# Kernel optimization log

Hardware: AMD Instinct MI355X
Metric: run time of the kernel (lower is better)

Reference implementation:

```python
import jax, jax.numpy as jnp
import numpy as np

DIM = 384
HEADS = 12
K = 3          # kernel_size
PAD = 1
STRIDE = 1
B, H, W = 8, 56, 56


def conv1x1(x, w, b=None):
    # x: [B,C,H,W], w: [O,C]
    y = jnp.einsum('bchw,oc->bohw', x, w)
    if b is not None:
        y = y + b[None, :, None, None]
    return y


def unfold(x, k, p, s):
    # torch nn.Unfold: returns patches [B, C, k*k, nH, nW], kernel row-major, channel-major overall
    Bx, C, Hx, Wx = x.shape
    nH = (Hx + 2 * p - k) // s + 1
    nW = (Wx + 2 * p - k) // s + 1
    xp = jnp.pad(x, ((0, 0), (0, 0), (p, p), (p, p)))
    cols = [xp[:, :, i:i + s * nH:s, j:j + s * nW:s] for i in range(k) for j in range(k)]
    return jnp.stack(cols, axis=2), nH, nW


def fold(col, Hx, Wx, k, p, s):
    # torch F.fold (col2im): scatter-add overlapping windows. col: [B, C, k*k, nH, nW]
    Bx, C, _, nH, nW = col.shape
    canvas = jnp.zeros((Bx, C, Hx + 2 * p, Wx + 2 * p), col.dtype)
    idx = 0
    for i in range(k):
        for j in range(k):
            canvas = canvas.at[:, :, i:i + s * nH:s, j:j + s * nW:s].add(col[:, :, idx])
            idx += 1
    return canvas[:, :, p:p + Hx, p:p + Wx]


def setup_inputs() -> dict:
    key = jax.random.key(0)
    ks = jax.random.split(key, 5)
    k2 = K * K
    x = jax.random.normal(ks[0], (B, DIM, H, W), dtype=jnp.float32)
    v_w = jax.random.normal(ks[1], (DIM, DIM), dtype=jnp.float32) * 0.02
    v_b = jnp.zeros((DIM,), dtype=jnp.float32)
    attn_w = jax.random.normal(ks[2], (k2 * k2 * HEADS, DIM), dtype=jnp.float32) * 0.02
    proj_w = jax.random.normal(ks[3], (DIM, DIM), dtype=jnp.float32) * 0.02
    return {'x': x, 'v_w': v_w, 'v_b': v_b, 'attn_w': attn_w, 'proj_w': proj_w}


def reference(x, v_w, v_b, attn_w, proj_w):
    Bx, C, Hx, Wx = x.shape
    k2 = K * K
    hd = C // HEADS  # head dim
    # value projection + unfold into overlapping k x k windows
    v = conv1x1(x, v_w, v_b)
    vcol, nH, nW = unfold(v, K, PAD, STRIDE)        # [B, C, k2, nH, nW]
    L = nH * nW
    v = vcol.reshape(Bx, HEADS, hd, k2, L)          # split C = (heads, hd), heads slow
    v = v.transpose(0, 1, 4, 3, 2)                  # [B, n, L, k2(d), hd]
    # adaptive avg pool to (nH, nW); with stride=1 this is identity (pool window 1)
    ph, pw = Hx // nH, Wx // nW
    xp = x.reshape(Bx, C, nH, ph, nW, pw).mean(axis=(3, 5))
    # per-pixel attention logits, channel layout = ((i*k2 + d)*HEADS + head)
    a = jnp.einsum('bchw,oc->bohw', xp, attn_w)     # [B, k2*k2*n, nH, nW]
    a = a.reshape(Bx, k2, k2, HEADS, L)             # [B, i, d, n, L]
    a = a.transpose(0, 3, 4, 1, 2)                  # [B, n, L, i, d]
    a = jax.nn.softmax(a, axis=-1)
    out = jnp.einsum('bnlid,bnldh->bnlih', a, v)    # [B, n, L, i, hd]
    out = out.transpose(0, 1, 4, 3, 2)              # [B, n, hd, i, L] -> channel (n*hd+h)
    out = out.reshape(Bx, C, k2, nH, nW)
    out = fold(out, Hx, Wx, K, PAD, STRIDE)         # scatter-add windows back
    return conv1x1(out, proj_w)
```

## Files before the change

### kernel.cpp

```cpp
#include <hip/hip_runtime.h>
#include <hip/hip_bf16.h>

#define DIM   384
#define HEADS 12
#define K2    9
#define HH    56
#define WW    56
#define HWP   3136
#define BB    8
#define AO    972
#define AOP   1024
#define MCAT  1408
#define PP    3200

typedef __hip_bfloat16 bf16;
typedef short bf16x8 __attribute__((ext_vector_type(8)));
typedef short bf16x4v __attribute__((ext_vector_type(4)));
typedef float f32x4 __attribute__((ext_vector_type(4)));

static __device__ __forceinline__ float b2f(bf16 v) { return __bfloat162float(v); }
static __device__ __forceinline__ float bs2f(short s) {
    return __uint_as_float(((unsigned int)(unsigned short)s) << 16);
}
static __device__ __forceinline__ short f2bs(float f) {
    __hip_bfloat16 h = __float2bfloat16(f);
    return *(short*)&h;
}

static __device__ __forceinline__ void gl_lds16(const bf16* g, bf16* l) {
    __builtin_amdgcn_global_load_lds(
        (const __attribute__((address_space(1))) unsigned int*)g,
        (__attribute__((address_space(3))) unsigned int*)l, 16, 0, 0);
}

__global__ __launch_bounds__(256) void prep_kernel(
        const float* __restrict__ x, const float* __restrict__ v_w,
        const float* __restrict__ attn_w, const float* __restrict__ proj_w,
        bf16* __restrict__ xT, bf16* __restrict__ wcat, bf16* __restrict__ wp) {
    const int bid = blockIdx.x;
    if (bid < 400) {
        const int lane = threadIdx.x & 63, w = threadIdx.x >> 6;
        const int p = (bid % 50) * 64 + lane;
        const int b = bid / 50;
        bf16* dst = xT + ((size_t)b * PP + p) * DIM;
        if (p >= HWP) {
            bf16x8 z = {};
            for (int cg = w; cg < 48; cg += 4) *(bf16x8*)(dst + cg * 8) = z;
            return;
        }
        const float* src = x + (size_t)b * DIM * HWP + p;
        for (int cg = w; cg < 48; cg += 4) {
            bf16x8 v;
#pragma unroll
            for (int j = 0; j < 8; j++) v[j] = f2bs(src[(size_t)(cg * 8 + j) * HWP]);
            *(bf16x8*)(dst + cg * 8) = v;
        }
    } else {
        const int idx = (bid - 400) * 256 + threadIdx.x;
        const int NCAT = MCAT * DIM;
        if (idx < NCAT) {
            const int row = idx / DIM, col = idx % DIM;
            float v;
            if (row < 384) v = v_w[row * DIM + col];
            else { const int r2 = row - 384; v = (r2 < AO) ? attn_w[r2 * DIM + col] : 0.f; }
            *(short*)&wcat[idx] = f2bs(v);
        } else {
            const int j = idx - NCAT;
            if (j < 384 * DIM) *(short*)&wp[j] = f2bs(proj_w[j]);
        }
    }
}

#define GEMM_MAIN_LOOP_V4(Ab, Bb, lA, lB, acc)                                 \
    for (int k0 = 0; k0 < DIM; k0 += 64) {                                     \
        _Pragma("unroll")                                                      \
        for (int r = 0; r < 4; r++) {                                          \
            int idx = r * 256 + t;                                             \
            int row = idx >> 3;                                                \
            int kq = ((idx & 7) - (row >> 1)) & 7;                             \
            gl_lds16(Ab + (size_t)row * DIM + k0 + kq * 8, lA + idx * 8);      \
        }                                                                      \
        _Pragma("unroll")                                                      \
        for (int r = 0; r < 4; r++) {                                          \
            int idx = r * 256 + t;                                             \
            int row = idx >> 3;                                                \
            int kq = ((idx & 7) - (row >> 1)) & 7;                             \
            gl_lds16(Bb + (size_t)row * DIM + k0 + kq * 8, lB + idx * 8);      \
        }                                                                      \
        __syncthreads();                                                       \
        _Pragma("unroll")                                                      \
        for (int h = 0; h < 2; h++) {                                          \
            const int swzh = (((h << 2) + quad + (l16 >> 1)) & 7) * 8;         \
            bf16x8 af[4], bfr[4];                                              \
            _Pragma("unroll")                                                  \
            for (int mt = 0; mt < 4; mt++)                                     \
                af[mt] = *(const bf16x8*)(lA + (wm * 64 + mt * 16 + l16) * 64 + swzh); \
            _Pragma("unroll")                                                  \
            for (int nt = 0; nt < 4; nt++)                                     \
                bfr[nt] = *(const bf16x8*)(lB + (wn * 64 + nt * 16 + l16) * 64 + swzh); \
            _Pragma("unroll")                                                  \
            for (int mt = 0; mt < 4; mt++)                                     \
                _Pragma("unroll")                                              \
                for (int nt = 0; nt < 4; nt++)                                 \
                    acc[mt][nt] = __builtin_amdgcn_mfma_f32_16x16x32_bf16(     \
                        af[mt], bfr[nt], acc[mt][nt], 0, 0, 0);                \
        }                                                                      \
        __syncthreads();                                                       \
    }

__global__ __launch_bounds__(256) void gemm12_kernel(
        const bf16* __restrict__ A, const bf16* __restrict__ Bt,
        const float* __restrict__ bias, bf16* __restrict__ vT,
        bf16* __restrict__ lT) {
    __shared__ bf16 lds[16384];
    bf16* lA = lds;
    bf16* lB = lds + 8192;
    const int t = threadIdx.x;
    const int lane = t & 63, w = t >> 6;
    const int wm = w & 1, wn = w >> 1;
    const int quad = lane >> 4, l16 = lane & 15;
    const int n0 = blockIdx.x * 128;
    const int m0 = blockIdx.y * 128;
    const int b = blockIdx.z;

    const bf16* Ab = A + (size_t)m0 * DIM;
    const bf16* Bb = Bt + ((size_t)b * PP + n0) * DIM;

    f32x4 acc[4][4] = {};
    GEMM_MAIN_LOOP_V4(Ab, Bb, lA, lB, acc)

    const bool isv = (m0 < 384);
    bf16* outp = isv ? vT : lT;
    const int ostr = isv ? DIM : AOP;
    const int ch0 = isv ? m0 : m0 - 384;

    bf16* wbuf = lds + w * 1152;
    const int nr = lane >> 2;
    const int mc = (lane & 3) * 16;
#pragma unroll
    for (int nt = 0; nt < 4; nt++) {
#pragma unroll
        for (int mt = 0; mt < 4; mt++) {
            float4 bi = make_float4(0.f, 0.f, 0.f, 0.f);
            if (isv) bi = *(const float4*)(bias + ch0 + wm * 64 + mt * 16 + quad * 4);
            bf16x4v pk;
            pk[0] = f2bs(acc[mt][nt][0] + bi.x);
            pk[1] = f2bs(acc[mt][nt][1] + bi.y);
            pk[2] = f2bs(acc[mt][nt][2] + bi.z);
            pk[3] = f2bs(acc[mt][nt][3] + bi.w);
            *(bf16x4v*)(wbuf + l16 * 72 + mt * 16 + quad * 4) = pk;
        }
        bf16x8 v0 = *(const bf16x8*)(wbuf + nr * 72 + mc);
        bf16x8 v1 = *(const bf16x8*)(wbuf + nr * 72 + mc + 8);
        const int p = n0 + wn * 64 + nt * 16 + nr;
        if (p < HWP) {
            bf16* dp = outp + ((size_t)b * PP + p) * ostr + ch0 + wm * 64 + mc;
            *(bf16x8*)dp = v0;
            *(bf16x8*)(dp + 8) = v1;
        }
    }
}

__global__ __launch_bounds__(256) void gemm_planar_kernel(
        const bf16* __restrict__ A, const bf16* __restrict__ Bt,
        float* __restrict__ out) {
    __shared__ bf16 lds[16384];
    bf16* lA = lds;
    bf16* lB = lds + 8192;
    const int t = threadIdx.x;
    const int lane = t & 63, w = t >> 6;
    const int wm = w & 1, wn = w >> 1;
    const int quad = lane >> 4, l16 = lane & 15;
    const int n0 = blockIdx.x * 128;
    const int m0 = blockIdx.y * 128;
    const int b = blockIdx.z;

    const bf16* Ab = A + (size_t)m0 * DIM;
    const bf16* Bb = Bt + ((size_t)b * PP + n0) * DIM;

    f32x4 acc[4][4] = {};
    GEMM_MAIN_LOOP_V4(Ab, Bb, lA, lB, acc)

#pragma unroll
    for (int mt = 0; mt < 4; mt++) {
#pragma unroll
        for (int nt = 0; nt < 4; nt++) {
            int p = n0 + wn * 64 + nt * 16 + l16;
            if (p >= HWP) continue;
#pragma unroll
            for (int reg = 0; reg < 4; reg++) {
                int o = m0 + wm * 64 + mt * 16 + quad * 4 + reg;
                out[((size_t)b * DIM + o) * HWP + p] = acc[mt][nt][reg];
            }
        }
    }
}

__global__ __launch_bounds__(384) void attn_fold_kernel(
        const bf16* __restrict__ lT, const bf16* __restrict__ vT,
        bf16* __restrict__ cT) {
    __shared__ bf16 P[8 * 9 * 12 * 9];
    __shared__ float Wf[8 * 25 * 12];
    const int t = threadIdx.x;
    const int b = blockIdx.y;
    const int pix0 = blockIdx.x * 8;
    const int Y = pix0 / WW, X0 = pix0 % WW;

    for (int r = t; r < 864; r += 384) {
        const int px = r / 108, rem = r % 108;
        const int i = rem / 12, n = rem % 12;
        const int ir = i / 3, ic = i % 3;
        const int yi = Y + 1 - ir, xi = X0 + px + 1 - ic;
        bf16* Pd = &P[r * 9];
        if (yi < 0 || yi >= HH || xi < 0 || xi >= WW) {
#pragma unroll
            for (int d = 0; d < K2; d++) *(short*)&Pd[d] = 0;
        } else {
            const bf16* base = lT + ((size_t)b * PP + yi * WW + xi) * AOP + i * 108 + n;
            float lv[K2];
            float m = -1e30f;
#pragma unroll
            for (int d = 0; d < K2; d++) {
                lv[d] = b2f(base[d * 12]);
                m = fmaxf(m, lv[d]);
            }
            float s = 0.f;
#pragma unroll
            for (int d = 0; d < K2; d++) { lv[d] = __expf(lv[d] - m); s += lv[d]; }
            const float inv = 1.f / s;
#pragma unroll
            for (int d = 0; d < K2; d++) *(short*)&Pd[d] = f2bs(lv[d] * inv);
        }
    }
    __syncthreads();

    for (int e = t; e < 2400; e += 384) {
        const int px = e / 300, rem = e % 300;
        const int off = rem / 12, n = rem % 12;
        const int dy = off / 5 - 2, dx = off % 5 - 2;
        const int ir_lo = max(0, -dy), ir_hi = min(2, 2 - dy);
        const int ic_lo = max(0, -dx), ic_hi = min(2, 2 - dx);
        float wsum = 0.f;
        for (int ir = ir_lo; ir <= ir_hi; ir++)
            for (int ic = ic_lo; ic <= ic_hi; ic++) {
                const int i = ir * 3 + ic;
                const int d = (dy + ir) * 3 + (dx + ic);
                wsum += b2f(P[((px * 9 + i) * 12 + n) * 9 + d]);
            }
        Wf[e] = wsum;
    }
    __syncthreads();

    const int px = t / 48, cg = t % 48;
    const int X = X0 + px;
    const int n = cg >> 2;
    const float* Wp = &Wf[px * 300];
    const bf16* vb = vT + (size_t)b * PP * DIM;
    float acc[8] = {};
#pragma unroll
    for (int dy = -2; dy <= 2; dy++) {
        const int ny = Y + dy;
        if (ny < 0 || ny >= HH) continue;
#pragma unroll
        for (int dx = -2; dx <= 2; dx++) {
            const int nx = X + dx;
            const bool ok = (nx >= 0 && nx < WW);
            const int nxc = min(max(nx, 0), WW - 1);
            const float w = ok ? Wp[((dy + 2) * 5 + dx + 2) * 12 + n] : 0.f;
            bf16x8 vv = *(const bf16x8*)(vb + (size_t)(ny * WW + nxc) * DIM + cg * 8);
#pragma unroll
            for (int j = 0; j < 8; j++) acc[j] += w * bs2f(vv[j]);
        }
    }
    bf16x8 po;
#pragma unroll
    for (int j = 0; j < 8; j++) po[j] = f2bs(acc[j]);
    *(bf16x8*)(cT + ((size_t)b * PP + pix0 + px) * DIM + cg * 8) = po;
}

extern "C" void kernel_launch(void* const* d_in, const int* in_sizes, int n_in,
                              void* d_out, int out_size, void* d_ws, size_t ws_size,
                              hipStream_t stream) {
    const float* x      = (const float*)d_in[0];
    const float* v_w    = (const float*)d_in[1];
    const float* v_b    = (const float*)d_in[2];
    const float* attn_w = (const float*)d_in[3];
    const float* proj_w = (const float*)d_in[4];
    float* out = (float*)d_out;

    bf16* xT    = (bf16*)d_ws;
    bf16* vT    = xT + (size_t)BB * PP * DIM;
    bf16* lT    = vT + (size_t)BB * PP * DIM;
    bf16* wcat  = lT + (size_t)BB * PP * AOP;
    bf16* wp    = wcat + (size_t)MCAT * DIM;
    bf16* cT    = xT;

    const int NW = MCAT * DIM + 384 * DIM;
    const int nprep = 400 + (NW + 255) / 256;
    prep_kernel<<<nprep, 256, 0, stream>>>(x, v_w, attn_w, proj_w, xT, wcat, wp);

    gemm12_kernel<<<dim3(PP / 128, MCAT / 128, BB), 256, 0, stream>>>(wcat, xT, v_b, vT, lT);
    attn_fold_kernel<<<dim3(HWP / 8, BB), 384, 0, stream>>>(lT, vT, cT);
    gemm_planar_kernel<<<dim3(PP / 128, 3, BB), 256, 0, stream>>>(wp, cT, out);
}
```

Measured before the change: 217.8 us.

## Store value tensor in zero-padded 60x60 layout to remove fold boundary checks

```diff
diff --git a/kernel.cpp b/kernel.cpp
--- a/kernel.cpp
+++ b/kernel.cpp
@@ -12,11 +12,17 @@
 #define AOP   1024
 #define MCAT  1408
 #define PP    3200
+#define PPAD  3600
+#define W60   60
+
+#define WBLK     2688
+#define HALOBLK  696
 
 typedef __hip_bfloat16 bf16;
 typedef short bf16x8 __attribute__((ext_vector_type(8)));
 typedef short bf16x4v __attribute__((ext_vector_type(4)));
 typedef float f32x4 __attribute__((ext_vector_type(4)));
+typedef float f32x2 __attribute__((ext_vector_type(2)));
 
 static __device__ __forceinline__ float b2f(bf16 v) { return __bfloat162float(v); }
 static __device__ __forceinline__ float bs2f(short s) {
@@ -25,6 +31,12 @@
 static __device__ __forceinline__ short f2bs(float f) {
     __hip_bfloat16 h = __float2bfloat16(f);
     return *(short*)&h;
+}
+static __device__ __forceinline__ f32x2 unpk(unsigned int u) {
+    f32x2 r;
+    r[0] = __uint_as_float(u << 16);
+    r[1] = __uint_as_float(u & 0xffff0000u);
+    return r;
 }
 
 static __device__ __forceinline__ void gl_lds16(const bf16* g, bf16* l) {
@@ -36,7 +48,8 @@
 __global__ __launch_bounds__(256) void prep_kernel(
         const float* __restrict__ x, const float* __restrict__ v_w,
         const float* __restrict__ attn_w, const float* __restrict__ proj_w,
-        bf16* __restrict__ xT, bf16* __restrict__ wcat, bf16* __restrict__ wp) {
+        bf16* __restrict__ xT, bf16* __restrict__ wcat, bf16* __restrict__ wp,
+        bf16* __restrict__ vP) {
     const int bid = blockIdx.x;
     if (bid < 400) {
         const int lane = threadIdx.x & 63, w = threadIdx.x >> 6;
@@ -55,7 +68,7 @@
             for (int j = 0; j < 8; j++) v[j] = f2bs(src[(size_t)(cg * 8 + j) * HWP]);
             *(bf16x8*)(dst + cg * 8) = v;
         }
-    } else {
+    } else if (bid < 400 + WBLK) {
         const int idx = (bid - 400) * 256 + threadIdx.x;
         const int NCAT = MCAT * DIM;
         if (idx < NCAT) {
@@ -68,6 +81,24 @@
             const int j = idx - NCAT;
             if (j < 384 * DIM) *(short*)&wp[j] = f2bs(proj_w[j]);
         }
+    } else {
+        const int hidx = (bid - 400 - WBLK) * 256 + threadIdx.x;
+        const int b = hidx / 22272;
+        const int r = hidx % 22272;
+        const int hp = r / 48, cgi = r % 48;
+        int row, col;
+        if (hp < 240) {
+            const int rr = hp / 60;
+            row = (rr < 2) ? rr : rr + 56;
+            col = hp % 60;
+        } else {
+            const int h2 = hp - 240;
+            row = 2 + (h2 >> 2);
+            const int c4 = h2 & 3;
+            col = (c4 < 2) ? c4 : c4 + 56;
+        }
+        bf16x8 z = {};
+        *(bf16x8*)(vP + ((size_t)b * PPAD + row * W60 + col) * DIM + cgi * 8) = z;
     }
 }
 
@@ -110,7 +141,7 @@
 
 __global__ __launch_bounds__(256) void gemm12_kernel(
         const bf16* __restrict__ A, const bf16* __restrict__ Bt,
-        const float* __restrict__ bias, bf16* __restrict__ vT,
+        const float* __restrict__ bias, bf16* __restrict__ vP,
         bf16* __restrict__ lT) {
     __shared__ bf16 lds[16384];
     bf16* lA = lds;
@@ -130,8 +161,6 @@
     GEMM_MAIN_LOOP_V4(Ab, Bb, lA, lB, acc)
 
     const bool isv = (m0 < 384);
-    bf16* outp = isv ? vT : lT;
-    const int ostr = isv ? DIM : AOP;
     const int ch0 = isv ? m0 : m0 - 384;
 
     bf16* wbuf = lds + w * 1152;
@@ -154,7 +183,13 @@
         bf16x8 v1 = *(const bf16x8*)(wbuf + nr * 72 + mc + 8);
         const int p = n0 + wn * 64 + nt * 16 + nr;
         if (p < HWP) {
-            bf16* dp = outp + ((size_t)b * PP + p) * ostr + ch0 + wm * 64 + mc;
+            bf16* dp;
+            if (isv) {
+                const int y = p / WW;
+                dp = vP + ((size_t)b * PPAD + p + y * 4 + 122) * DIM + ch0 + wm * 64 + mc;
+            } else {
+                dp = lT + ((size_t)b * PP + p) * AOP + ch0 + wm * 64 + mc;
+            }
             *(bf16x8*)dp = v0;
             *(bf16x8*)(dp + 8) = v1;
         }
@@ -197,7 +232,7 @@
 }
 
 __global__ __launch_bounds__(384) void attn_fold_kernel(
-        const bf16* __restrict__ lT, const bf16* __restrict__ vT,
+        const bf16* __restrict__ lT, const bf16* __restrict__ vP,
         bf16* __restrict__ cT) {
     __shared__ bf16 P[8 * 9 * 12 * 9];
     __shared__ float Wf[8 * 25 * 12];
@@ -234,47 +269,52 @@
     }
     __syncthreads();
 
-    for (int e = t; e < 2400; e += 384) {
-        const int px = e / 300, rem = e % 300;
-        const int off = rem / 12, n = rem % 12;
+    if (t < 300) {
+        const int off = t / 12, n = t % 12;
         const int dy = off / 5 - 2, dx = off % 5 - 2;
         const int ir_lo = max(0, -dy), ir_hi = min(2, 2 - dy);
         const int ic_lo = max(0, -dx), ic_hi = min(2, 2 - dx);
-        float wsum = 0.f;
-        for (int ir = ir_lo; ir <= ir_hi; ir++)
-            for (int ic = ic_lo; ic <= ic_hi; ic++) {
-                const int i = ir * 3 + ic;
-                const int d = (dy + ir) * 3 + (dx + ic);
-                wsum += b2f(P[((px * 9 + i) * 12 + n) * 9 + d]);
-            }
-        Wf[e] = wsum;
+#pragma unroll
+        for (int px = 0; px < 8; px++) {
+            float wsum = 0.f;
+            for (int ir = ir_lo; ir <= ir_hi; ir++)
+                for (int ic = ic_lo; ic <= ic_hi; ic++) {
+                    const int i = ir * 3 + ic;
+                    const int d = (dy + ir) * 3 + (dx + ic);
+                    wsum += b2f(P[((px * 9 + i) * 12 + n) * 9 + d]);
+                }
+            Wf[(px * 25 + off) * 12 + n] = wsum;
+        }
     }
     __syncthreads();
 
     const int px = t / 48, cg = t % 48;
     const int X = X0 + px;
     const int n = cg >> 2;
-    const float* Wp = &Wf[px * 300];
-    const bf16* vb = vT + (size_t)b * PP * DIM;
-    float acc[8] = {};
+    const float* Wp = &Wf[px * 300 + n];
+    const bf16* vbp = vP + ((size_t)b * PPAD + (size_t)(Y + 2) * W60 + (X + 2)) * DIM + cg * 8;
+    f32x2 a2[4] = {};
 #pragma unroll
     for (int dy = -2; dy <= 2; dy++) {
-        const int ny = Y + dy;
-        if (ny < 0 || ny >= HH) continue;
+        const bf16* rowb = vbp + dy * (W60 * DIM);
+        const float* wrow = Wp + (dy + 2) * 60;
 #pragma unroll
         for (int dx = -2; dx <= 2; dx++) {
-            const int nx = X + dx;
-            const bool ok = (nx >= 0 && nx < WW);
-            const int nxc = min(max(nx, 0), WW - 1);
-            const float w = ok ? Wp[((dy + 2) * 5 + dx + 2) * 12 + n] : 0.f;
-            bf16x8 vv = *(const bf16x8*)(vb + (size_t)(ny * WW + nxc) * DIM + cg * 8);
-#pragma unroll
-            for (int j = 0; j < 8; j++) acc[j] += w * bs2f(vv[j]);
+            const float w = wrow[(dx + 2) * 12];
+            const uint4 d = *(const uint4*)(rowb + dx * DIM);
+            f32x2 w2; w2[0] = w; w2[1] = w;
+            a2[0] = __builtin_elementwise_fma(unpk(d.x), w2, a2[0]);
+            a2[1] = __builtin_elementwise_fma(unpk(d.y), w2, a2[1]);
+            a2[2] = __builtin_elementwise_fma(unpk(d.z), w2, a2[2]);
+            a2[3] = __builtin_elementwise_fma(unpk(d.w), w2, a2[3]);
         }
     }
     bf16x8 po;
 #pragma unroll
-    for (int j = 0; j < 8; j++) po[j] = f2bs(acc[j]);
+    for (int j = 0; j < 4; j++) {
+        po[2 * j]     = f2bs(a2[j][0]);
+        po[2 * j + 1] = f2bs(a2[j][1]);
+    }
     *(bf16x8*)(cT + ((size_t)b * PP + pix0 + px) * DIM + cg * 8) = po;
 }
 
@@ -289,17 +329,16 @@
     float* out = (float*)d_out;
 
     bf16* xT    = (bf16*)d_ws;
-    bf16* vT    = xT + (size_t)BB * PP * DIM;
-    bf16* lT    = vT + (size_t)BB * PP * DIM;
+    bf16* vP    = xT + (size_t)BB * PP * DIM;
+    bf16* lT    = vP + (size_t)BB * PPAD * DIM;
     bf16* wcat  = lT + (size_t)BB * PP * AOP;
     bf16* wp    = wcat + (size_t)MCAT * DIM;
     bf16* cT    = xT;
 
-    const int NW = MCAT * DIM + 384 * DIM;
-    const int nprep = 400 + (NW + 255) / 256;
-    prep_kernel<<<nprep, 256, 0, stream>>>(x, v_w, attn_w, proj_w, xT, wcat, wp);
-
-    gemm12_kernel<<<dim3(PP / 128, MCAT / 128, BB), 256, 0, stream>>>(wcat, xT, v_b, vT, lT);
-    attn_fold_kernel<<<dim3(HWP / 8, BB), 384, 0, stream>>>(lT, vT, cT);
+    const int nprep = 400 + WBLK + HALOBLK;
+    prep_kernel<<<nprep, 256, 0, stream>>>(x, v_w, attn_w, proj_w, xT, wcat, wp, vP);
+
+    gemm12_kernel<<<dim3(PP / 128, MCAT / 128, BB), 256, 0, stream>>>(wcat, xT, v_b, vP, lT);
+    attn_fold_kernel<<<dim3(HWP / 8, BB), 384, 0, stream>>>(lT, vP, cT);
     gemm_planar_kernel<<<dim3(PP / 128, 3, BB), 256, 0, stream>>>(wp, cT, out);
 }
```

New measurement: 217.4 us. No clear change (-0.2%).
